# Performance work log

Hardware: AMD Instinct MI355X
Metric: run time of the kernel (lower is better)

Reference implementation:

```python
import jax, jax.numpy as jnp
import numpy as np

THETA = 10000.0
AXES_DIM = (16, 56, 56)  # sums to head_dim=128
HEADS = 24
HEAD_DIM = 128
EPS = 1e-5


def _pos_embed(ids):
    # ids: (S, n_axes) int -> cos, sin each (S, head_dim//2)
    pos = ids.astype(jnp.float32)
    cos_out, sin_out = [], []
    for i, d in enumerate(AXES_DIM):
        freqs = 1.0 / (THETA ** (jnp.arange(0, d, 2, dtype=jnp.float32) / d))  # (d/2,)
        ang = pos[:, i][:, None] * freqs[None, :]  # (S, d/2)
        cos_out.append(jnp.cos(ang))
        sin_out.append(jnp.sin(ang))
    return jnp.concatenate(cos_out, -1), jnp.concatenate(sin_out, -1)


def _rms_norm(x, w):
    # per-head RMSNorm over last dim (head_dim)
    var = jnp.mean(x * x, axis=-1, keepdims=True)
    return x * jax.lax.rsqrt(var + EPS) * w


def _apply_rope(x, cos, sin):
    # non-neox (interleaved) rotary. x: (B,S,H,D), cos/sin: (S,D/2)
    x1 = x[..., 0::2]
    x2 = x[..., 1::2]
    c = cos[None, :, None, :]
    s = sin[None, :, None, :]
    o1 = x1 * c - x2 * s
    o2 = x2 * c + x1 * s
    return jnp.stack([o1, o2], axis=-1).reshape(x.shape)


def setup_inputs() -> dict:
    key = jax.random.key(0)
    ks = jax.random.split(key, 12)
    B, S_img, S_txt, D = 1, 2048, 512, 3072
    sd = 1.0 / np.sqrt(D)
    return {
        "hidden_states": jax.random.normal(ks[0], (B, S_img, D), jnp.float32),
        "encoder_hidden_states": jax.random.normal(ks[1], (B, S_txt, D), jnp.float32),
        "ids": jax.random.randint(ks[2], (S_txt + S_img, 3), 0, 64, jnp.int32),
        "w_qkv": jax.random.normal(ks[3], (D, 3 * D), jnp.float32) * sd,
        "w_add_qkv": jax.random.normal(ks[4], (D, 3 * D), jnp.float32) * sd,
        "b_add_qkv": jax.random.normal(ks[5], (3 * D,), jnp.float32) * 0.02,
        "w_out": jax.random.normal(ks[6], (D, D), jnp.float32) * sd,
        "b_out": jax.random.normal(ks[7], (D,), jnp.float32) * 0.02,
        "w_add_out": jax.random.normal(ks[8], (D, D), jnp.float32) * sd,
        "b_add_out": jax.random.normal(ks[9], (D,), jnp.float32) * 0.02,
        "norm_q_w": jnp.ones((HEAD_DIM,), jnp.float32),
        "norm_k_w": jnp.ones((HEAD_DIM,), jnp.float32),
        "norm_add_q_w": jnp.ones((HEAD_DIM,), jnp.float32),
        "norm_add_k_w": jnp.ones((HEAD_DIM,), jnp.float32),
    }


def reference(hidden_states, encoder_hidden_states, ids, w_qkv, w_add_qkv,
              b_add_qkv, w_out, b_out, w_add_out, b_add_out,
              norm_q_w, norm_k_w, norm_add_q_w, norm_add_k_w):
    B, S_img, D = hidden_states.shape
    S_txt = encoder_hidden_states.shape[1]
    H, Dh = HEADS, HEAD_DIM

    # fused QKV projections
    qkv = hidden_states @ w_qkv  # (B, S_img, 3D)
    q, k, v = jnp.split(qkv, 3, axis=-1)
    q = _rms_norm(q.reshape(B, S_img, H, Dh), norm_q_w)
    k = _rms_norm(k.reshape(B, S_img, H, Dh), norm_k_w)
    v = v.reshape(B, S_img, H, Dh)

    eqkv = encoder_hidden_states @ w_add_qkv + b_add_qkv
    eq, ek, ev = jnp.split(eqkv, 3, axis=-1)
    eq = _rms_norm(eq.reshape(B, S_txt, H, Dh), norm_add_q_w)
    ek = _rms_norm(ek.reshape(B, S_txt, H, Dh), norm_add_k_w)
    ev = ev.reshape(B, S_txt, H, Dh)

    # joint sequence: text first, then image
    q = jnp.concatenate([eq, q], axis=1)
    k = jnp.concatenate([ek, k], axis=1)
    v = jnp.concatenate([ev, v], axis=1)

    # multi-axis RoPE over joint positions
    cos, sin = _pos_embed(ids)  # (S_txt+S_img, Dh/2)
    q = _apply_rope(q, cos, sin)
    k = _apply_rope(k, cos, sin)

    # scaled dot-product attention (non-causal)
    scale = 1.0 / np.sqrt(Dh)
    scores = jnp.einsum("bqhd,bkhd->bhqk", q, k) * scale
    probs = jax.nn.softmax(scores, axis=-1)
    attn = jnp.einsum("bhqk,bkhd->bqhd", probs, v)
    attn = attn.reshape(B, S_txt + S_img, H * Dh)

    enc_out = attn[:, :S_txt] @ w_add_out + b_add_out
    img_out = attn[:, S_txt:] @ w_out + b_out
    return img_out, enc_out
```

## Files before the change

kernel.cpp:

```cpp
#include <hip/hip_runtime.h>

typedef __attribute__((ext_vector_type(8))) short short8;
typedef __attribute__((ext_vector_type(4))) short short4v;
typedef __attribute__((ext_vector_type(4))) float floatx4;

__device__ __forceinline__ float b2f(short b) {
  union { unsigned u; float f; } v; v.u = ((unsigned)(unsigned short)b) << 16; return v.f;
}
__device__ __forceinline__ short f2b(float f) {
  union { float f; unsigned u; } v; v.f = f;
  return (short)((v.u + 0x7fffu + ((v.u >> 16) & 1u)) >> 16);
}
__device__ __forceinline__ unsigned cvtpk(float lo, float hi) {
  unsigned r;
  asm("v_cvt_pk_bf16_f32 %0, %1, %2" : "=v"(r) : "v"(lo), "v"(hi));
  return r;
}
__device__ __forceinline__ float loadf(const void* p, size_t i, bool f32) {
  return f32 ? ((const float*)p)[i] : b2f(((const short*)p)[i]);
}
__device__ __forceinline__ short8 load8(const void* p, size_t i, bool f32) {
  if (f32) {
    const float* fp = (const float*)p + i;
    float4 a = *(const float4*)fp;
    float4 b = *(const float4*)(fp + 4);
    short8 r;
    r[0] = f2b(a.x); r[1] = f2b(a.y); r[2] = f2b(a.z); r[3] = f2b(a.w);
    r[4] = f2b(b.x); r[5] = f2b(b.y); r[6] = f2b(b.z); r[7] = f2b(b.w);
    return r;
  }
  return *(const short8*)((const short*)p + i);
}

__device__ __forceinline__ void gload16(const short* g, short* l) {
  __builtin_amdgcn_global_load_lds(
      (const __attribute__((address_space(1))) unsigned int*)g,
      (__attribute__((address_space(3))) unsigned int*)l, 16, 0, 0);
}

__global__ void detect_dtype(const unsigned short* __restrict__ w, int* __restrict__ flag) {
  __shared__ int cnt;
  if (threadIdx.x == 0) cnt = 0;
  __syncthreads();
  int bad = 0;
  for (int i = threadIdx.x; i < 4096; i += 256) {
    int e = (w[i] >> 7) & 0xFF;
    if (e >= 0xC8) bad++;
  }
  atomicAdd(&cnt, bad);
  __syncthreads();
  if (threadIdx.x == 0) *flag = (cnt > 64) ? 1 : 0;
}

__global__ __launch_bounds__(256)
void cvt_bf16_2(const void* __restrict__ srcA, long n8A,
                const void* __restrict__ srcB, long n8B,
                short* __restrict__ dst, const int* __restrict__ dflag) {
  const bool f32 = (*dflag != 0);
  const long n8 = n8A + n8B;
  long stride = (long)gridDim.x * 256;
  for (long i = (long)blockIdx.x * 256 + threadIdx.x; i < n8; i += stride) {
    const void* s; long e;
    if (i < n8A) { s = srcA; e = i * 8; } else { s = srcB; e = (i - n8A) * 8; }
    if (f32) {
      const float* fp = (const float*)s + e;
      float4 a = *(const float4*)fp;
      float4 b = *(const float4*)(fp + 4);
      short8 r;
      r[0] = f2b(a.x); r[1] = f2b(a.y); r[2] = f2b(a.z); r[3] = f2b(a.w);
      r[4] = f2b(b.x); r[5] = f2b(b.y); r[6] = f2b(b.z); r[7] = f2b(b.w);
      *(short8*)(dst + i * 8) = r;
    } else {
      *(short8*)(dst + i * 8) = *(const short8*)((const short*)s + e);
    }
  }
}

__global__ __launch_bounds__(256)
void cvt_t2(const void* __restrict__ src0, short* __restrict__ dst0,
            const void* __restrict__ src1, short* __restrict__ dst1,
            int K, int N, const int* __restrict__ dflag) {
  __shared__ short st[64][72];
  const bool f32 = (*dflag != 0);
  const void* src = blockIdx.z ? src1 : src0;
  short* dst = blockIdx.z ? dst1 : dst0;
  const int n0 = blockIdx.x << 6, k0 = blockIdx.y << 6;
  const int c4 = threadIdx.x & 15;
  const int rq = threadIdx.x >> 4;
#pragma unroll
  for (int r = 0; r < 4; ++r) {
    int k = r * 16 + rq;
    int n = c4 * 4;
    short v0, v1, v2, v3;
    if (f32) {
      const float* sp = (const float*)src + (size_t)(k0 + k) * N + n0 + n;
      float4 f = *(const float4*)sp;
      v0 = f2b(f.x); v1 = f2b(f.y); v2 = f2b(f.z); v3 = f2b(f.w);
    } else {
      const short* sp = (const short*)src + (size_t)(k0 + k) * N + n0 + n;
      short4v s = *(const short4v*)sp;
      v0 = s[0]; v1 = s[1]; v2 = s[2]; v3 = s[3];
    }
    st[n + 0][k] = v0; st[n + 1][k] = v1; st[n + 2][k] = v2; st[n + 3][k] = v3;
  }
  __syncthreads();
  const int n = threadIdx.x >> 2;
  const int kc = (threadIdx.x & 3) << 4;
  short8 a = *(const short8*)(&st[n][kc]);
  short8 b = *(const short8*)(&st[n][kc + 8]);
  short* dp = dst + (size_t)(n0 + n) * K + k0 + kc;
  *(short8*)(dp) = a;
  *(short8*)(dp + 8) = b;
}

__global__ __launch_bounds__(256, 2)
void gemm_bt(const void* __restrict__ A, int a_row0,
             const void* __restrict__ B, const void* __restrict__ bias,
             void* __restrict__ C, int c_row0, int N, int K,
             const int* __restrict__ dflag, int aIn, int cOut) {
  __shared__ short As[128 * 32];
  __shared__ short Bs[128 * 32];
  const bool f32 = (*dflag != 0);
  const bool a32 = aIn && f32;
  const bool c32 = cOut && f32;
  const int tid = threadIdx.x;
  const int lane = tid & 63, w = tid >> 6;
  const int wm = w & 1, wn = w >> 1;
  const int qg = lane >> 4, l16 = lane & 15;
  const int m0 = blockIdx.y << 7, n0 = blockIdx.x << 7;

  const int arow = tid >> 2, ak = (tid & 3) << 3;
  const int brow = tid >> 4, bc = (tid & 15) << 3;
  const int rot = tid & 15;

  floatx4 acc[4][4];
#pragma unroll
  for (int i = 0; i < 4; ++i)
#pragma unroll
    for (int j = 0; j < 4; ++j) acc[i][j] = (floatx4){0.f, 0.f, 0.f, 0.f};

  for (int k0 = 0; k0 < K; k0 += 32) {
    __syncthreads();
#pragma unroll
    for (int j = 0; j < 2; ++j) {
      short8 av = load8(A, (size_t)(a_row0 + m0 + j * 64 + arow) * K + (k0 + ak), a32);
      *(short8*)(As + (j * 64 + arow) * 32 + ak) = av;
      int kr = j * 16 + brow;
      short8 bv = load8(B, (size_t)(k0 + kr) * N + (n0 + bc), f32);
      int kq = kr >> 3, kj = kr & 7;
#pragma unroll
      for (int s = 0; s < 8; ++s) {
        int u = (s + rot) & 7;
        int n = bc + u;
        Bs[(n << 5) + ((kq ^ (n & 3)) << 3) + kj] = bv[u];
      }
    }
    __syncthreads();
    short8 a[4];
#pragma unroll
    for (int mi = 0; mi < 4; ++mi)
      a[mi] = *(const short8*)(As + (wm * 64 + mi * 16 + l16) * 32 + qg * 8);
#pragma unroll
    for (int ni = 0; ni < 4; ++ni) {
      int n = wn * 64 + ni * 16 + l16;
      short8 b = *(const short8*)(Bs + (n << 5) + ((qg ^ (n & 3)) << 3));
#pragma unroll
      for (int mi = 0; mi < 4; ++mi)
        acc[mi][ni] = __builtin_amdgcn_mfma_f32_16x16x32_bf16(a[mi], b, acc[mi][ni], 0, 0, 0);
    }
  }
#pragma unroll
  for (int ni = 0; ni < 4; ++ni) {
    int col = n0 + wn * 64 + ni * 16 + l16;
    float bv = bias ? loadf(bias, col, f32) : 0.0f;
#pragma unroll
    for (int mi = 0; mi < 4; ++mi) {
      int row = m0 + wm * 64 + mi * 16 + qg * 4;
#pragma unroll
      for (int r = 0; r < 4; ++r) {
        size_t idx = (size_t)(c_row0 + row + r) * N + col;
        float val = acc[mi][ni][r] + bv;
        if (c32) ((float*)C)[idx] = val;
        else     ((short*)C)[idx] = f2b(val);
      }
    }
  }
}

__global__ __launch_bounds__(256, 3)
void gemm_bf2(const short* __restrict__ A,
              const short* __restrict__ BTa, const void* __restrict__ biasa,
              int a0a, int c0a, int nYa,
              const short* __restrict__ BTb, const void* __restrict__ biasb,
              int a0b, int c0b,
              void* __restrict__ C, int N, int K,
              const int* __restrict__ dflag, int cOut) {
  __shared__ short As[3][128 * 32];
  __shared__ short Bs[3][128 * 32];
  const bool f32 = (*dflag != 0);
  const bool c32 = cOut && f32;
  const int y = blockIdx.y;
  const short* BT; const void* bias; int arow0, crow0;
  if (y < nYa) { BT = BTa; bias = biasa; arow0 = a0a + (y << 7); crow0 = c0a + (y << 7); }
  else { int my = y - nYa; BT = BTb; bias = biasb; arow0 = a0b + (my << 7); crow0 = c0b + (my << 7); }
  const int tid = threadIdx.x;
  const int lane = tid & 63, w = tid >> 6;
  const int wm = w & 1, wn = w >> 1;
  const int qg = lane >> 4, l16 = lane & 15;
  const int n0 = blockIdx.x << 7;
  const int garow = lane >> 2;
  const int gcir = lane & 3;
  const int nk = K >> 5;
  const int swz = (gcir ^ (garow & 3) ^ (garow >> 2)) << 3;
  const short* Abase = A + (size_t)(arow0 + w * 32 + garow) * K + swz;
  const short* Bbase = BT + (size_t)(n0 + w * 32 + garow) * K + swz;
  const int rswz = (l16 & 3) ^ (l16 >> 2);

  floatx4 acc[4][4];
#pragma unroll
  for (int i = 0; i < 4; ++i)
#pragma unroll
    for (int j = 0; j < 4; ++j) acc[i][j] = (floatx4){0.f, 0.f, 0.f, 0.f};

  auto STAGE = [&](int buf, int k0) {
#pragma unroll
    for (int j = 0; j < 2; ++j) {
      gload16(Abase + (size_t)j * 16 * K + k0, &As[buf][(w * 2 + j) << 9]);
      gload16(Bbase + (size_t)j * 16 * K + k0, &Bs[buf][(w * 2 + j) << 9]);
    }
  };

  STAGE(0, 0);
  if (nk > 1) STAGE(1, 32);

  int cb = 0;
  for (int t = 0; t < nk; ++t) {
    if (t + 1 < nk) {
      asm volatile("s_waitcnt vmcnt(4) lgkmcnt(0)" ::: "memory");
    } else {
      asm volatile("s_waitcnt vmcnt(0) lgkmcnt(0)" ::: "memory");
    }
    __builtin_amdgcn_s_barrier();
    if (t + 2 < nk) {
      int sb = (cb == 0) ? 2 : cb - 1;
      STAGE(sb, (t + 2) << 5);
    }
    short8 a[4], b[4];
#pragma unroll
    for (int mi = 0; mi < 4; ++mi) {
      int ra = wm * 64 + mi * 16 + l16;
      a[mi] = *(const short8*)(&As[cb][(ra << 5) + ((qg ^ rswz) << 3)]);
    }
#pragma unroll
    for (int ni = 0; ni < 4; ++ni) {
      int n = wn * 64 + ni * 16 + l16;
      b[ni] = *(const short8*)(&Bs[cb][(n << 5) + ((qg ^ rswz) << 3)]);
    }
    __builtin_amdgcn_s_setprio(1);
#pragma unroll
    for (int ni = 0; ni < 4; ++ni)
#pragma unroll
      for (int mi = 0; mi < 4; ++mi)
        acc[mi][ni] = __builtin_amdgcn_mfma_f32_16x16x32_bf16(a[mi], b[ni], acc[mi][ni], 0, 0, 0);
    __builtin_amdgcn_s_setprio(0);
    cb = (cb == 2) ? 0 : cb + 1;
  }
#pragma unroll
  for (int ni = 0; ni < 4; ++ni) {
    int col = n0 + wn * 64 + ni * 16 + l16;
    float bvv = bias ? loadf(bias, col, f32) : 0.0f;
#pragma unroll
    for (int mi = 0; mi < 4; ++mi) {
      int row = wm * 64 + mi * 16 + qg * 4;
#pragma unroll
      for (int r = 0; r < 4; ++r) {
        size_t idx = (size_t)(crow0 + row + r) * N + col;
        float val = acc[mi][ni][r] + bvv;
        if (c32) ((float*)C)[idx] = val;
        else     ((short*)C)[idx] = f2b(val);
      }
    }
  }
}

__global__ __launch_bounds__(512)
void norm_rope(short* __restrict__ qkv, const int* __restrict__ ids,
               const void* __restrict__ nqw, const void* __restrict__ nkw,
               const void* __restrict__ naqw, const void* __restrict__ nakw,
               const int* __restrict__ dflag) {
  const bool f32 = (*dflag != 0);
  const int t = blockIdx.x, wv = threadIdx.x >> 6, lane = threadIdx.x & 63;
  const bool txt = t < 512;
  int p = lane, axis; float expo;
  if (p < 8)       { axis = 0; expo = (float)(2 * p) * (1.0f / 16.0f); }
  else if (p < 36) { axis = 1; expo = (float)(2 * (p - 8)) * (1.0f / 56.0f); }
  else             { axis = 2; expo = (float)(2 * (p - 36)) * (1.0f / 56.0f); }
  float freq = __expf(-expo * 9.210340371976184f);
  float ang = (float)ids[t * 3 + axis] * freq;
  float s, c; sincosf(ang, &s, &c);
  const void* qw = txt ? naqw : nqw;
  const void* kw = txt ? nakw : nkw;
  float w0q = loadf(qw, 2 * lane, f32), w1q = loadf(qw, 2 * lane + 1, f32);
  float w0k = loadf(kw, 2 * lane, f32), w1k = loadf(kw, 2 * lane + 1, f32);
  const float QS = 0.08838834764831845f * 1.4426950408889634f;
#pragma unroll
  for (int i = 0; i < 3; ++i) {
    int h = wv + 8 * i;
    short* qp = qkv + (size_t)t * 9216 + h * 128 + 2 * lane;
    short* kp = qp + 3072;
    union { unsigned u; short sh[2]; } qv, kv;
    qv.u = *(const unsigned*)qp;
    kv.u = *(const unsigned*)kp;
    float q0 = b2f(qv.sh[0]), q1 = b2f(qv.sh[1]);
    float k0 = b2f(kv.sh[0]), k1 = b2f(kv.sh[1]);
    float sq = q0 * q0 + q1 * q1, sk = k0 * k0 + k1 * k1;
#pragma unroll
    for (int o = 1; o < 64; o <<= 1) { sq += __shfl_xor(sq, o); sk += __shfl_xor(sk, o); }
    float rq = rsqrtf(sq * (1.0f / 128.0f) + 1e-5f);
    float rk = rsqrtf(sk * (1.0f / 128.0f) + 1e-5f);
    float qn0 = q0 * rq * w0q, qn1 = q1 * rq * w1q;
    float kn0 = k0 * rk * w0k, kn1 = k1 * rk * w1k;
    float qo0 = qn0 * c - qn1 * s, qo1 = qn1 * c + qn0 * s;
    float ko0 = kn0 * c - kn1 * s, ko1 = kn1 * c + kn0 * s;
    union { unsigned u; short sh[2]; } qo, ko;
    qo.sh[0] = f2b(qo0 * QS);
    qo.sh[1] = f2b(qo1 * QS);
    ko.sh[0] = f2b(ko0); ko.sh[1] = f2b(ko1);
    *(unsigned*)qp = qo.u;
    *(unsigned*)kp = ko.u;
  }
}

__global__ __launch_bounds__(512, 2)
void attn_fa(const short* __restrict__ qkv, short* __restrict__ attn) {
  __shared__ short QPs[256 * 128];
  __shared__ short KVs[2][128 * 128];
  const int wgid = blockIdx.x;
  const int xcd = wgid & 7, slot = wgid >> 3;
  const int h = xcd * 3 + slot / 10;
  const int qt = slot % 10;
  const int tid = threadIdx.x, lane = tid & 63, w = tid >> 6;
  const int qg = lane >> 4, l16 = lane & 15;
  const int lr = lane >> 4, lc = lane & 15;
  const int q0 = qt << 8;
  const int sc = tid & 15;
  const int srow5 = (tid >> 4) & 15, half = tid >> 8;

  const short* Qg  = qkv + (size_t)q0 * 9216 + h * 128;
  const short* Kg0 = qkv + 3072 + h * 128;
  const short* Vg0 = qkv + 6144 + h * 128;

  short8 vr[4];
#pragma unroll
  for (int j = 0; j < 8; ++j) {
    int row = j * 32 + w * 4 + lr;
    gload16(Qg + (size_t)row * 9216 + ((lc ^ (row & 7)) << 3),
            QPs + (j * 32 + w * 4) * 128);
  }
#pragma unroll
  for (int j = 0; j < 4; ++j) {
    int row = j * 32 + w * 4 + lr;
    gload16(Kg0 + (size_t)row * 9216 + ((lc ^ (row & 7)) << 3),
            &KVs[0][(j * 32 + w * 4) * 128]);
  }
#pragma unroll
  for (int j = 0; j < 4; ++j) {
    int row = half * 64 + j * 16 + srow5;
    vr[j] = *(const short8*)(Vg0 + (size_t)row * 9216 + sc * 8);
  }
  asm volatile("s_waitcnt vmcnt(8) lgkmcnt(0)" ::: "memory");
  __builtin_amdgcn_s_barrier();
  short8 aq[2][4];
#pragma unroll
  for (int mi = 0; mi < 2; ++mi)
#pragma unroll
    for (int kc = 0; kc < 4; ++kc) {
      int row = w * 32 + mi * 16 + l16;
      aq[mi][kc] = *(const short8*)(QPs + row * 128 + (((kc * 4 + qg) ^ (row & 7)) << 3));
    }

  floatx4 acc_o[2][8];
#pragma unroll
  for (int mi = 0; mi < 2; ++mi)
#pragma unroll
    for (int nd = 0; nd < 8; ++nd) acc_o[mi][nd] = (floatx4){0.f, 0.f, 0.f, 0.f};
  float m_i[2][4], l_i[2][4];
#pragma unroll
  for (int mi = 0; mi < 2; ++mi)
#pragma unroll
    for (int r = 0; r < 4; ++r) { m_i[mi][r] = -1e30f; l_i[mi][r] = 0.0f; }

  for (int kt = 0; kt < 20; ++kt) {
    const int c = kt & 1;
    asm volatile("s_waitcnt vmcnt(4) lgkmcnt(0)" ::: "memory");
    __builtin_amdgcn_s_barrier();
    if (kt < 19) {
      const short* Kg = qkv + ((size_t)(kt + 1) * 128) * 9216 + 3072 + h * 128;
#pragma unroll
      for (int j = 0; j < 4; ++j) {
        int row = j * 32 + w * 4 + lr;
        gload16(Kg + (size_t)row * 9216 + ((lc ^ (row & 7)) << 3),
                &KVs[1 - c][(j * 32 + w * 4) * 128]);
      }
    }
    floatx4 acc_s[2][8];
#pragma unroll
    for (int mi = 0; mi < 2; ++mi)
#pragma unroll
      for (int ni = 0; ni < 8; ++ni) acc_s[mi][ni] = (floatx4){0.f, 0.f, 0.f, 0.f};
    __builtin_amdgcn_s_setprio(1);
#pragma unroll
    for (int kc = 0; kc < 4; ++kc) {
#pragma unroll
      for (int ni = 0; ni < 8; ++ni) {
        int row = ni * 16 + l16;
        short8 b = *(const short8*)(&KVs[c][row * 128 + (((kc * 4 + qg) ^ (row & 7)) << 3)]);
        acc_s[0][ni] = __builtin_amdgcn_mfma_f32_16x16x32_bf16(aq[0][kc], b, acc_s[0][ni], 0, 0, 0);
        acc_s[1][ni] = __builtin_amdgcn_mfma_f32_16x16x32_bf16(aq[1][kc], b, acc_s[1][ni], 0, 0, 0);
      }
    }
    __builtin_amdgcn_s_setprio(0);
    float mxv[2][4];
    bool need = false;
#pragma unroll
    for (int mi = 0; mi < 2; ++mi) {
#pragma unroll
      for (int r = 0; r < 4; ++r) {
        float mx = acc_s[mi][0][r];
#pragma unroll
        for (int ni = 1; ni < 8; ++ni) mx = fmaxf(mx, acc_s[mi][ni][r]);
        mx = fmaxf(mx, __shfl_xor(mx, 1));
        mx = fmaxf(mx, __shfl_xor(mx, 2));
        mx = fmaxf(mx, __shfl_xor(mx, 4));
        mx = fmaxf(mx, __shfl_xor(mx, 8));
        mxv[mi][r] = mx;
        need = need || (mx > m_i[mi][r] + 8.0f);
      }
    }
    if (__ballot(need)) {
#pragma unroll
      for (int mi = 0; mi < 2; ++mi) {
#pragma unroll
        for (int r = 0; r < 4; ++r) {
          float mn = fmaxf(m_i[mi][r], mxv[mi][r]);
          float al = __builtin_amdgcn_exp2f(m_i[mi][r] - mn);
          m_i[mi][r] = mn;
          l_i[mi][r] *= al;
#pragma unroll
          for (int nd = 0; nd < 8; ++nd) acc_o[mi][nd][r] *= al;
        }
      }
    }
#pragma unroll
    for (int mi = 0; mi < 2; ++mi) {
      float rs[4] = {0.f, 0.f, 0.f, 0.f};
#pragma unroll
      for (int r = 0; r < 4; ++r) {
        float pv[8];
#pragma unroll
        for (int ni = 0; ni < 8; ++ni) {
          pv[ni] = __builtin_amdgcn_exp2f(acc_s[mi][ni][r] - m_i[mi][r]);
          rs[r] += pv[ni];
        }
        unsigned u0 = cvtpk(pv[0], pv[1]);
        unsigned u1 = cvtpk(pv[2], pv[3]);
        unsigned u2 = cvtpk(pv[4], pv[5]);
        unsigned u3 = cvtpk(pv[6], pv[7]);
        int row = w * 32 + mi * 16 + qg * 4 + r;
        uint4 uu; uu.x = u0; uu.y = u1; uu.z = u2; uu.w = u3;
        *(uint4*)(QPs + row * 128 + ((l16 ^ (row & 15)) << 3)) = uu;
      }
#pragma unroll
      for (int r = 0; r < 4; ++r) {
        float t = rs[r];
        t += __shfl_xor(t, 1); t += __shfl_xor(t, 2);
        t += __shfl_xor(t, 4); t += __shfl_xor(t, 8);
        l_i[mi][r] += t;
      }
    }
    asm volatile("s_waitcnt lgkmcnt(0)" ::: "memory");
    __builtin_amdgcn_s_barrier();
#pragma unroll
    for (int u = 0; u < 8; ++u) {
      int d = sc * 8 + u;
      short4v pk = { vr[0][u], vr[1][u], vr[2][u], vr[3][u] };
      *(short4v*)(&KVs[c][d * 128 + (((srow5 ^ u ^ (sc & 7))) << 3) + half * 4]) = pk;
    }
    if (kt < 19) {
      const short* Vg = qkv + ((size_t)(kt + 1) * 128) * 9216 + 6144 + h * 128;
#pragma unroll
      for (int j = 0; j < 4; ++j) {
        int row = half * 64 + j * 16 + srow5;
        vr[j] = *(const short8*)(Vg + (size_t)row * 9216 + sc * 8);
      }
    }
    asm volatile("s_waitcnt lgkmcnt(0)" ::: "memory");
    __builtin_amdgcn_s_barrier();
    __builtin_amdgcn_s_setprio(1);
#pragma unroll
    for (int kc = 0; kc < 4; ++kc) {
      int prow0 = w * 32 + l16;
      short8 ap0 = *(const short8*)(QPs + prow0 * 128 + (((kc * 4 + qg) ^ (prow0 & 15)) << 3));
      int prow1 = prow0 + 16;
      short8 ap1 = *(const short8*)(QPs + prow1 * 128 + (((kc * 4 + qg) ^ (prow1 & 15)) << 3));
#pragma unroll
      for (int nd = 0; nd < 8; ++nd) {
        int row = nd * 16 + l16;
        int chn = (kc * 4 + qg) ^ (row & 7) ^ ((row >> 3) & 7);
        short8 b = *(const short8*)(&KVs[c][row * 128 + (chn << 3)]);
        acc_o[0][nd] = __builtin_amdgcn_mfma_f32_16x16x32_bf16(ap0, b, acc_o[0][nd], 0, 0, 0);
        acc_o[1][nd] = __builtin_amdgcn_mfma_f32_16x16x32_bf16(ap1, b, acc_o[1][nd], 0, 0, 0);
      }
    }
    __builtin_amdgcn_s_setprio(0);
  }
#pragma unroll
  for (int mi = 0; mi < 2; ++mi) {
    float inv[4];
#pragma unroll
    for (int r = 0; r < 4; ++r) inv[r] = 1.0f / l_i[mi][r];
#pragma unroll
    for (int nd = 0; nd < 8; ++nd) {
#pragma unroll
      for (int r = 0; r < 4; ++r) {
        int row = w * 32 + mi * 16 + qg * 4 + r;
        QPs[row * 128 + nd * 16 + l16] = f2b(acc_o[mi][nd][r] * inv[r]);
      }
    }
  }
  asm volatile("s_waitcnt lgkmcnt(0)" ::: "memory");
#pragma unroll
  for (int j = 0; j < 8; ++j) {
    int rrow = w * 32 + j * 4 + qg;
    short8 vv = *(const short8*)(QPs + rrow * 128 + l16 * 8);
    *(short8*)(attn + (size_t)(q0 + rrow) * 3072 + h * 128 + l16 * 8) = vv;
  }
}

extern "C" void kernel_launch(void* const* d_in, const int* in_sizes, int n_in,
                              void* d_out, int out_size, void* d_ws, size_t ws_size,
                              hipStream_t stream) {
  (void)in_sizes; (void)n_in; (void)out_size;
  const void* hidden    = d_in[0];
  const void* enc       = d_in[1];
  const int*  ids       = (const int*)d_in[2];
  const void* w_qkv     = d_in[3];
  const void* w_add_qkv = d_in[4];
  const void* b_add_qkv = d_in[5];
  const void* w_out     = d_in[6];
  const void* b_out     = d_in[7];
  const void* w_add_out = d_in[8];
  const void* b_add_out = d_in[9];
  const void* nqw  = d_in[10];
  const void* nkw  = d_in[11];
  const void* naqw = d_in[12];
  const void* nakw = d_in[13];

  int*   dflag = (int*)d_ws;
  short* qkv   = (short*)((char*)d_ws + 256);
  short* attnB = qkv + (size_t)2560 * 9216;

  short* pool  = attnB + (size_t)2560 * 3072;
  const long n_hid  = 2048L * 3072;
  const long n_enc  = 512L * 3072;
  const long n_wqkv = 3072L * 9216;
  const long n_wout = 3072L * 3072;
  short* xb   = pool;
  short* wqb  = xb + n_enc + n_hid;
  short* waqb = wqb + n_wqkv;
  short* wob  = waqb + n_wqkv;
  short* waob = wob + n_wout;
  const size_t REQ = 256 + 2 * ((size_t)2560 * 9216 + (size_t)2560 * 3072 +
                                n_hid + n_enc + 2 * n_wqkv + 2 * n_wout);

  detect_dtype<<<1, 256, 0, stream>>>((const unsigned short*)w_qkv, dflag);

  if (ws_size >= REQ) {
    cvt_bf16_2<<<1024, 256, 0, stream>>>(enc, n_enc / 8, hidden, n_hid / 8, xb, dflag);
    cvt_t2<<<dim3(144, 48, 2), 256, 0, stream>>>(w_qkv, wqb, w_add_qkv, waqb, 3072, 9216, dflag);
    cvt_t2<<<dim3(48, 48, 2), 256, 0, stream>>>(w_out, wob, w_add_out, waob, 3072, 3072, dflag);

    gemm_bf2<<<dim3(72, 20), 256, 0, stream>>>(
        xb, waqb, b_add_qkv, 0, 0, 4, wqb, nullptr, 512, 512,
        qkv, 9216, 3072, dflag, 0);
    norm_rope<<<dim3(2560), 512, 0, stream>>>(qkv, ids, nqw, nkw, naqw, nakw, dflag);
    attn_fa<<<dim3(240), 512, 0, stream>>>(qkv, attnB);
    gemm_bf2<<<dim3(24, 20), 256, 0, stream>>>(
        attnB, wob, b_out, 512, 0, 16, waob, b_add_out, 0, 2048,
        d_out, 3072, 3072, dflag, 1);
  } else {
    gemm_bt<<<dim3(72, 4), 256, 0, stream>>>(enc, 0, w_add_qkv, b_add_qkv, qkv, 0, 9216, 3072, dflag, 1, 0);
    gemm_bt<<<dim3(72, 16), 256, 0, stream>>>(hidden, 0, w_qkv, nullptr, qkv, 512, 9216, 3072, dflag, 1, 0);
    norm_rope<<<dim3(2560), 512, 0, stream>>>(qkv, ids, nqw, nkw, naqw, nakw, dflag);
    attn_fa<<<dim3(240), 512, 0, stream>>>(qkv, attnB);
    gemm_bt<<<dim3(24, 16), 256, 0, stream>>>(attnB, 512, w_out, b_out, d_out, 0, 3072, 3072, dflag, 0, 1);
    gemm_bt<<<dim3(24, 4), 256, 0, stream>>>(attnB, 0, w_add_out, b_add_out, d_out, 2048, 3072, 3072, dflag, 0, 1);
  }
}
```

Measured before the change: 840.6 us.

## Merge weight transpose kernels, remap GEMM blocks, stage epilogue through LDS

The two weight-transpose launches become one flat-grid kernel, saving a launch. The GEMM remaps its flat block index with a stride-8 permutation, likely so neighbouring blocks land on the same XCD and share L2. The GEMM epilogue now writes results through LDS so each wave stores contiguous 16-byte rows instead of scattered 2- or 4-byte stores. This costs extra LDS traffic and barriers, and the remap assumes the block count divides by 8.

```diff
diff --git a/kernel.cpp b/kernel.cpp
--- a/kernel.cpp
+++ b/kernel.cpp
@@ -77,14 +77,28 @@
 }
 
 __global__ __launch_bounds__(256)
-void cvt_t2(const void* __restrict__ src0, short* __restrict__ dst0,
-            const void* __restrict__ src1, short* __restrict__ dst1,
-            int K, int N, const int* __restrict__ dflag) {
+void cvt_tw(const void* __restrict__ wq, short* __restrict__ wqd,
+            const void* __restrict__ waq, short* __restrict__ waqd,
+            const void* __restrict__ wo, short* __restrict__ wod,
+            const void* __restrict__ wao, short* __restrict__ waod,
+            const int* __restrict__ dflag) {
   __shared__ short st[64][72];
   const bool f32 = (*dflag != 0);
-  const void* src = blockIdx.z ? src1 : src0;
-  short* dst = blockIdx.z ? dst1 : dst0;
-  const int n0 = blockIdx.x << 6, k0 = blockIdx.y << 6;
+  const int K = 3072;
+  int b = blockIdx.x;
+  const void* src; short* dst; int N, n0, k0;
+  if (b < 13824) {
+    src = (b < 6912) ? wq : waq;
+    dst = (b < 6912) ? wqd : waqd;
+    int rem = b % 6912;
+    N = 9216; n0 = (rem % 144) << 6; k0 = (rem / 144) << 6;
+  } else {
+    b -= 13824;
+    src = (b < 2304) ? wo : wao;
+    dst = (b < 2304) ? wod : waod;
+    int rem = b % 2304;
+    N = 3072; n0 = (rem % 48) << 6; k0 = (rem / 48) << 6;
+  }
   const int c4 = threadIdx.x & 15;
   const int rq = threadIdx.x >> 4;
 #pragma unroll
@@ -107,10 +121,10 @@
   const int n = threadIdx.x >> 2;
   const int kc = (threadIdx.x & 3) << 4;
   short8 a = *(const short8*)(&st[n][kc]);
-  short8 b = *(const short8*)(&st[n][kc + 8]);
+  short8 bb = *(const short8*)(&st[n][kc + 8]);
   short* dp = dst + (size_t)(n0 + n) * K + k0 + kc;
   *(short8*)(dp) = a;
-  *(short8*)(dp + 8) = b;
+  *(short8*)(dp + 8) = bb;
 }
 
 __global__ __launch_bounds__(256, 2)
@@ -195,11 +209,16 @@
               int a0b, int c0b,
               void* __restrict__ C, int N, int K,
               const int* __restrict__ dflag, int cOut) {
-  __shared__ short As[3][128 * 32];
-  __shared__ short Bs[3][128 * 32];
+  __shared__ short Ls[6 * 128 * 32];
+#define ASB(b) (Ls + (b) * 4096)
+#define BSB(b) (Ls + (3 + (b)) * 4096)
   const bool f32 = (*dflag != 0);
   const bool c32 = cOut && f32;
-  const int y = blockIdx.y;
+  const int flat0 = blockIdx.y * gridDim.x + blockIdx.x;
+  const int nwg = gridDim.x * gridDim.y;
+  const int flat = (flat0 & 7) * (nwg >> 3) + (flat0 >> 3);
+  const int bx = flat % gridDim.x;
+  const int y = flat / gridDim.x;
   const short* BT; const void* bias; int arow0, crow0;
   if (y < nYa) { BT = BTa; bias = biasa; arow0 = a0a + (y << 7); crow0 = c0a + (y << 7); }
   else { int my = y - nYa; BT = BTb; bias = biasb; arow0 = a0b + (my << 7); crow0 = c0b + (my << 7); }
@@ -207,7 +226,7 @@
   const int lane = tid & 63, w = tid >> 6;
   const int wm = w & 1, wn = w >> 1;
   const int qg = lane >> 4, l16 = lane & 15;
-  const int n0 = blockIdx.x << 7;
+  const int n0 = bx << 7;
   const int garow = lane >> 2;
   const int gcir = lane & 3;
   const int nk = K >> 5;
@@ -225,8 +244,8 @@
   auto STAGE = [&](int buf, int k0) {
 #pragma unroll
     for (int j = 0; j < 2; ++j) {
-      gload16(Abase + (size_t)j * 16 * K + k0, &As[buf][(w * 2 + j) << 9]);
-      gload16(Bbase + (size_t)j * 16 * K + k0, &Bs[buf][(w * 2 + j) << 9]);
+      gload16(Abase + (size_t)j * 16 * K + k0, ASB(buf) + ((w * 2 + j) << 9));
+      gload16(Bbase + (size_t)j * 16 * K + k0, BSB(buf) + ((w * 2 + j) << 9));
     }
   };
 
@@ -249,12 +268,12 @@
 #pragma unroll
     for (int mi = 0; mi < 4; ++mi) {
       int ra = wm * 64 + mi * 16 + l16;
-      a[mi] = *(const short8*)(&As[cb][(ra << 5) + ((qg ^ rswz) << 3)]);
+      a[mi] = *(const short8*)(ASB(cb) + (ra << 5) + ((qg ^ rswz) << 3));
     }
 #pragma unroll
     for (int ni = 0; ni < 4; ++ni) {
       int n = wn * 64 + ni * 16 + l16;
-      b[ni] = *(const short8*)(&Bs[cb][(n << 5) + ((qg ^ rswz) << 3)]);
+      b[ni] = *(const short8*)(BSB(cb) + (n << 5) + ((qg ^ rswz) << 3));
     }
     __builtin_amdgcn_s_setprio(1);
 #pragma unroll
@@ -265,22 +284,53 @@
     __builtin_amdgcn_s_setprio(0);
     cb = (cb == 2) ? 0 : cb + 1;
   }
-#pragma unroll
-  for (int ni = 0; ni < 4; ++ni) {
-    int col = n0 + wn * 64 + ni * 16 + l16;
-    float bvv = bias ? loadf(bias, col, f32) : 0.0f;
-#pragma unroll
-    for (int mi = 0; mi < 4; ++mi) {
-      int row = wm * 64 + mi * 16 + qg * 4;
-#pragma unroll
-      for (int r = 0; r < 4; ++r) {
-        size_t idx = (size_t)(crow0 + row + r) * N + col;
-        float val = acc[mi][ni][r] + bvv;
-        if (c32) ((float*)C)[idx] = val;
-        else     ((short*)C)[idx] = f2b(val);
-      }
-    }
-  }
+  __builtin_amdgcn_s_barrier();
+  if (!c32) {
+    short* wreg = Ls + w * 4096;
+#pragma unroll
+    for (int ni = 0; ni < 4; ++ni) {
+      float bvv = bias ? loadf(bias, n0 + wn * 64 + ni * 16 + l16, f32) : 0.0f;
+#pragma unroll
+      for (int mi = 0; mi < 4; ++mi)
+#pragma unroll
+        for (int r = 0; r < 4; ++r)
+          wreg[(mi * 16 + qg * 4 + r) * 64 + ni * 16 + l16] = f2b(acc[mi][ni][r] + bvv);
+    }
+    asm volatile("s_waitcnt lgkmcnt(0)" ::: "memory");
+#pragma unroll
+    for (int j = 0; j < 8; ++j) {
+      int row = j * 8 + (lane >> 3);
+      int col = (lane & 7) * 8;
+      short8 v = *(const short8*)(wreg + row * 64 + col);
+      *(short8*)((short*)C + (size_t)(crow0 + wm * 64 + row) * N + n0 + wn * 64 + col) = v;
+    }
+  } else {
+    float* wregf = (float*)(Ls) + w * 2048;
+#pragma unroll
+    for (int half = 0; half < 2; ++half) {
+#pragma unroll
+      for (int nh = 0; nh < 2; ++nh) {
+        int ni = half * 2 + nh;
+        float bvv = bias ? loadf(bias, n0 + wn * 64 + ni * 16 + l16, f32) : 0.0f;
+#pragma unroll
+        for (int mi = 0; mi < 4; ++mi)
+#pragma unroll
+          for (int r = 0; r < 4; ++r)
+            wregf[(mi * 16 + qg * 4 + r) * 32 + nh * 16 + l16] = acc[mi][ni][r] + bvv;
+      }
+      asm volatile("s_waitcnt lgkmcnt(0)" ::: "memory");
+#pragma unroll
+      for (int j = 0; j < 8; ++j) {
+        int row = j * 8 + (lane >> 3);
+        int c4 = (lane & 7) * 4;
+        float4 v = *(const float4*)(wregf + row * 32 + c4);
+        *(float4*)((float*)C + (size_t)(crow0 + wm * 64 + row) * N + n0 + wn * 64 + half * 32 + c4) = v;
+      }
+      asm volatile("s_waitcnt lgkmcnt(0)" ::: "memory");
+    }
+  }
+#undef ASB
+#undef BSB
 }
 
 __global__ __launch_bounds__(512)
@@ -577,8 +627,8 @@
 
   if (ws_size >= REQ) {
     cvt_bf16_2<<<1024, 256, 0, stream>>>(enc, n_enc / 8, hidden, n_hid / 8, xb, dflag);
-    cvt_t2<<<dim3(144, 48, 2), 256, 0, stream>>>(w_qkv, wqb, w_add_qkv, waqb, 3072, 9216, dflag);
-    cvt_t2<<<dim3(48, 48, 2), 256, 0, stream>>>(w_out, wob, w_add_out, waob, 3072, 3072, dflag);
+    cvt_tw<<<dim3(18432), 256, 0, stream>>>(w_qkv, wqb, w_add_qkv, waqb,
+                                            w_out, wob, w_add_out, waob, dflag);
 
     gemm_bf2<<<dim3(72, 20), 256, 0, stream>>>(
         xb, waqb, b_add_qkv, 0, 0, 4, wqb, nullptr, 512, 512,
```

After: 823.4 us. 2.0% less time.
